# Kernel tuning notes

Hardware: AMD Instinct MI355X
Metric: run time of the kernel (lower is better)

The kernel has to match this reference:

```python
import jax, jax.numpy as jnp
import numpy as np

B, C, H, W = 4, 128, 56, 56
K = 7
K2 = K * K
RATIO = 16


def _conv1x1(x, w, b=None):
    # x: [B,C,H,W], w: [O,C]
    y = jnp.einsum('oc,bchw->bohw', w, x)
    return y if b is None else y + b[None, :, None, None]


def _dwconv(x, w, dil, pad):
    # depthwise conv, w: [C,1,k,k]
    return jax.lax.conv_general_dilated(
        x, w, window_strides=(1, 1), padding=[(pad, pad), (pad, pad)],
        rhs_dilation=(dil, dil), feature_group_count=x.shape[1],
        dimension_numbers=('NCHW', 'OIHW', 'NCHW'))


def _bn(x, s, b):
    # inference-mode BatchNorm folded to per-channel affine
    return x * s[None, :, None, None] + b[None, :, None, None]


def setup_inputs() -> dict:
    key = jax.random.key(0)
    ks = jax.random.split(key, 16)
    w = 0.05  # weight scale
    inp = {
        'x_up': jax.random.normal(ks[0], (B, C, H, W), jnp.float32),
        'x_skip': jax.random.normal(ks[1], (B, C, H, W), jnp.float32),
        'wq': jax.random.normal(ks[2], (C, C), jnp.float32) * w,
        'bq': jnp.zeros((C,), jnp.float32),
        'wk': jax.random.normal(ks[3], (C, C), jnp.float32) * w,
        'bk': jnp.zeros((C,), jnp.float32),
        'wv': jax.random.normal(ks[4], (C, C), jnp.float32) * w,
        'bv': jnp.zeros((C,), jnp.float32),
        'ww': jax.random.normal(ks[5], (K2, 49), jnp.float32) * w,
        'bw': jnp.zeros((K2,), jnp.float32),
        'lk_w': jax.random.normal(ks[6], (C, 1, K, K), jnp.float32) * 0.1,
        'lk_bn_s': jax.random.uniform(ks[7], (C,), jnp.float32, 0.5, 1.5),
        'lk_bn_b': jnp.zeros((C,), jnp.float32),
        'dw5': jax.random.normal(ks[8], (C, 1, 5, 5), jnp.float32) * 0.1,
        'bn5_s': jax.random.uniform(ks[7], (C,), jnp.float32, 0.5, 1.5),
        'bn5_b': jnp.zeros((C,), jnp.float32),
        'dw3a': jax.random.normal(ks[9], (C, 1, 3, 3), jnp.float32) * 0.1,
        'bn3a_s': jax.random.uniform(ks[9], (C,), jnp.float32, 0.5, 1.5),
        'bn3a_b': jnp.zeros((C,), jnp.float32),
        'dw3b': jax.random.normal(ks[10], (C, 1, 3, 3), jnp.float32) * 0.1,
        'bn3b_s': jax.random.uniform(ks[10], (C,), jnp.float32, 0.5, 1.5),
        'bn3b_b': jnp.zeros((C,), jnp.float32),
        'dw3c': jax.random.normal(ks[11], (C, 1, 3, 3), jnp.float32) * 0.1,
        'bn3c_s': jax.random.uniform(ks[11], (C,), jnp.float32, 0.5, 1.5),
        'bn3c_b': jnp.zeros((C,), jnp.float32),
        'lepe_bn_s': jax.random.uniform(ks[12], (C,), jnp.float32, 0.5, 1.5),
        'lepe_bn_b': jnp.zeros((C,), jnp.float32),
        'gate_w': jax.random.normal(ks[13], (C, C), jnp.float32) * w,
        'gate_bn_s': jax.random.uniform(ks[13], (C,), jnp.float32, 0.5, 1.5),
        'gate_bn_b': jnp.zeros((C,), jnp.float32),
        'fus_w': jax.random.normal(ks[14], (C, C), jnp.float32) * w,
        'fus_b': jnp.zeros((C,), jnp.float32),
        'ca_w1': jax.random.normal(ks[15], (C // RATIO, C), jnp.float32) * w,
        'ca_w2': jax.random.normal(ks[15], (C, C // RATIO), jnp.float32) * w,
        'res_scale': jnp.ones((1,), jnp.float32),
    }
    return inp


def _forward(x_up, x_skip, wq, bq, wk, bk, wv, bv, ww, bw,
             lk_w, lk_bn_s, lk_bn_b, dw5, bn5_s, bn5_b,
             dw3a, bn3a_s, bn3a_b, dw3b, bn3b_s, bn3b_b, dw3c, bn3c_s, bn3c_b,
             lepe_bn_s, lepe_bn_b, gate_w, gate_bn_s, gate_bn_b,
             fus_w, fus_b, ca_w1, ca_w2, res_scale):
    identity = x_skip

    # ---- lepe: DilatedReparamBlock (lk 7x7 dw + 4 dilated dw branches, each BN) + final BN
    out = _bn(_dwconv(x_skip, lk_w, 1, 3), lk_bn_s, lk_bn_b)
    out = out + _bn(_dwconv(x_skip, dw5, 1, 2), bn5_s, bn5_b)    # k=5, d=1
    out = out + _bn(_dwconv(x_skip, dw3a, 1, 1), bn3a_s, bn3a_b)  # k=3, d=1
    out = out + _bn(_dwconv(x_skip, dw3b, 2, 2), bn3b_s, bn3b_b)  # k=3, d=2
    out = out + _bn(_dwconv(x_skip, dw3c, 3, 3), bn3c_s, bn3c_b)  # k=3, d=3
    lepe = _bn(out, lepe_bn_s, lepe_bn_b)

    # ---- gate: 1x1 conv (no bias) -> BN -> SiLU
    gate = jax.nn.silu(_bn(_conv1x1(x_skip, gate_w), gate_bn_s, gate_bn_b))

    # ---- q / k / v
    query = _conv1x1(x_skip, wq, bq)                              # [B,C,H,W]
    # AdaptiveAvgPool2d(7): H,W divisible by 7 -> block mean
    pooled = x_up.reshape(B, C, 7, H // 7, 7, W // 7).mean(axis=(3, 5))  # [B,C,7,7]
    key_t = _conv1x1(pooled, wk, bk).reshape(B, C, 49)            # [B,C,49]
    value = _conv1x1(x_skip, wv, bv)                              # [B,C,H,W]

    # ---- attention over 49 pooled key tokens
    scale = float(C) ** -0.5
    q_r = query.reshape(B, C, H * W).transpose(0, 2, 1)           # [B,HW,C]
    attn = jax.nn.softmax(jnp.einsum('bnc,bcl->bnl', q_r, key_t) * scale, axis=-1)
    attn_r = attn.transpose(0, 2, 1).reshape(B, 49, H, W)         # [B,49,H,W]
    dyn_w = jnp.einsum('ol,blhw->bohw', ww, attn_r) + bw[None, :, None, None]  # [B,K2,H,W]

    # ---- unfold value (k=7, pad=3), torch layout: channel-major, (kh,kw) row-major
    pad = K // 2
    vp = jnp.pad(value, ((0, 0), (0, 0), (pad, pad), (pad, pad)))
    patches = jnp.stack([vp[:, :, i:i + H, j:j + W]
                         for i in range(K) for j in range(K)], axis=2)  # [B,C,K2,H,W]
    mixed = jnp.einsum('bkhw,bckhw->bchw', dyn_w, patches)

    x_fused = _conv1x1(mixed, fus_w, fus_b) + lepe

    # ---- channel attention (shared MLP on avg & max pooled)
    avg = x_fused.mean(axis=(2, 3))                               # [B,C]
    mx = x_fused.max(axis=(2, 3))                                 # [B,C]
    def ca_mlp(v):
        return jnp.einsum('cr,br->bc', ca_w2, jax.nn.relu(jnp.einsum('rc,bc->br', ca_w1, v)))
    ca = jax.nn.sigmoid(ca_mlp(avg) + ca_mlp(mx))[:, :, None, None]
    x_fused = ca * x_fused

    return gate * x_fused + identity * res_scale


def reference(x_up, x_skip, wq, bq, wk, bk, wv, bv, ww, bw,
              lk_w, lk_bn_s, lk_bn_b, dw5, bn5_s, bn5_b,
              dw3a, bn3a_s, bn3a_b, dw3b, bn3b_s, bn3b_b, dw3c, bn3c_s, bn3c_b,
              lepe_bn_s, lepe_bn_b, gate_w, gate_bn_s, gate_bn_b,
              fus_w, fus_b, ca_w1, ca_w2, res_scale):
    return _forward(x_up, x_skip, wq, bq, wk, bk, wv, bv, ww, bw,
                    lk_w, lk_bn_s, lk_bn_b, dw5, bn5_s, bn5_b,
                    dw3a, bn3a_s, bn3a_b, dw3b, bn3b_s, bn3b_b, dw3c, bn3c_s, bn3c_b,
                    lepe_bn_s, lepe_bn_b, gate_w, gate_bn_s, gate_bn_b,
                    fus_w, fus_b, ca_w1, ca_w2, res_scale)
```

## Files before the change

kernel.cpp:

```cpp
#include <hip/hip_runtime.h>

typedef unsigned int u32;

#define HW 3136
#define SCALE 0.08838834764831843f

#define OFF_W7    0
#define OFF_BIAS  6272
#define OFF_POOL  6400
#define OFF_MT    31488
#define OFF_D     56576
#define OFF_AVG   56772
#define OFF_MAXU  57284
#define OFF_CA    57796
#define OFF_WC    58308
#define OFF_BC    74692
#define OFF_FV    74820
#define OFF_GATE  1680452
#define OFF_DYN   3286084
#define OFF_XF    3900740

struct Params {
  const float *x_up, *x_skip, *wq, *bq, *wk, *bk, *wv, *bv, *ww, *bw;
  const float *lk_w, *lk_s, *lk_b, *dw5, *s5, *b5, *dw3a, *s3a, *b3a,
              *dw3b, *s3b, *b3b, *dw3c, *s3c, *b3c, *lepe_s, *lepe_b;
  const float *gate_w, *gate_s, *gate_b, *fus_w, *fus_b, *ca_w1, *ca_w2, *res;
  float* W;
  float* out;
};

__device__ __forceinline__ u32 fenc(float f){
  union{float f; u32 u;} v; v.f = f;
  return (v.u & 0x80000000u) ? ~v.u : (v.u | 0x80000000u);
}
__device__ __forceinline__ float fdec(u32 u){
  union{float f; u32 uu;} v;
  v.uu = (u & 0x80000000u) ? (u ^ 0x80000000u) : ~u;
  return v.f;
}

__global__ __launch_bounds__(256) void k_prep(Params P){
  __shared__ float pl[3136];
  __shared__ float part[208];
  float* W = P.W;
  const int tid = threadIdx.x, blk = blockIdx.x;
  if (blk < 512){
    const int b = blk >> 7, c = blk & 127;
    const float* src = P.x_up + (size_t)(b*128 + c)*HW;
    for (int idx = tid; idx < 784; idx += 256)
      *(float4*)&pl[idx*4] = *(const float4*)(src + idx*4);
    __syncthreads();
    if (tid < 196){
      const int l = tid >> 2, s = tid & 3;
      const int i = l/7, j = l%7;
      float sm = 0.f;
      #pragma unroll
      for (int r=0;r<2;++r){
        const int base = (8*i + 2*s + r)*56 + 8*j;
        #pragma unroll
        for (int e=0;e<8;++e) sm += pl[base+e];
      }
      part[tid] = sm;
    }
    __syncthreads();
    if (tid < 49){
      const float sm = part[tid*4] + part[tid*4+1] + part[tid*4+2] + part[tid*4+3];
      W[OFF_POOL + (size_t)(b*128+c)*49 + tid] = sm * (1.f/64.f);
    }
  } else if (blk < 576){
    const int o = (blk - 512)*2 + (tid >> 7), c = tid & 127;
    float a = 0.f;
    #pragma unroll 8
    for (int m=0;m<128;++m) a += P.fus_w[o*128+m] * P.wv[m*128+c];
    W[OFF_WC + o*128 + c] = a;
  } else if (blk == 576){
    for (int idx = tid; idx < 6272; idx += 256){
      const int c = idx/49, k = idx%49;
      const int dy = k/7 - 3, dx = k%7 - 3;
      float w = P.lk_s[c] * P.lk_w[c*49 + k];
      if (dy>=-2 && dy<=2 && dx>=-2 && dx<=2)
        w += P.s5[c] * P.dw5[c*25 + (dy+2)*5 + (dx+2)];
      if (dy>=-1 && dy<=1 && dx>=-1 && dx<=1)
        w += P.s3a[c] * P.dw3a[c*9 + (dy+1)*3 + (dx+1)];
      if ((dy==-2||dy==0||dy==2) && (dx==-2||dx==0||dx==2))
        w += P.s3b[c] * P.dw3b[c*9 + (dy/2+1)*3 + (dx/2+1)];
      if ((dy==-3||dy==0||dy==3) && (dx==-3||dx==0||dx==3))
        w += P.s3c[c] * P.dw3c[c*9 + (dy/3+1)*3 + (dx/3+1)];
      W[OFF_W7 + idx] = P.lepe_s[c] * w;
    }
    if (tid < 128){
      const float bs = P.lk_b[tid] + P.b5[tid] + P.b3a[tid] + P.b3b[tid] + P.b3c[tid];
      W[OFF_BIAS + tid] = P.lepe_s[tid] * bs + P.lepe_b[tid] + P.fus_b[tid];
    }
    for (int i = tid; i < 512; i += 256){
      W[OFF_AVG + i] = 0.f;
      ((u32*)W + OFF_MAXU)[i] = fenc(-1e30f);
    }
  } else {
    if (tid < 128){
      float a = 0.f;
      #pragma unroll 8
      for (int m=0;m<128;++m) a += P.fus_w[tid*128+m] * P.bv[m];
      W[OFF_BC + tid] = a;
    }
  }
}

__global__ __launch_bounds__(128) void k_key(Params P){
  __shared__ float pc[128], kc[128], red[128];
  float* W = P.W;
  const int b = blockIdx.x / 49, l = blockIdx.x % 49;
  const int t = threadIdx.x;
  pc[t] = W[OFF_POOL + (size_t)(b*128+t)*49 + l];
  __syncthreads();
  float acc = P.bk[t];
  const float4* wr = (const float4*)(P.wk + t*128);
  #pragma unroll 8
  for (int k0=0;k0<32;++k0){
    const float4 w = wr[k0];
    acc += w.x*pc[k0*4] + w.y*pc[k0*4+1] + w.z*pc[k0*4+2] + w.w*pc[k0*4+3];
  }
  kc[t] = acc;
  red[t] = P.bq[t] * acc;
  __syncthreads();
  float m = 0.f;
  #pragma unroll 8
  for (int c=0;c<128;++c) m += P.wq[c*128 + t] * kc[c];
  W[OFF_MT + (size_t)b*6272 + t*49 + l] = m * SCALE;
  if (t < 64) red[t] += red[t+64];
  __syncthreads();
  if (t < 32) red[t] += red[t+32];
  __syncthreads();
  if (t < 16) red[t] += red[t+16];
  __syncthreads();
  if (t < 8) red[t] += red[t+8];
  __syncthreads();
  if (t < 4) red[t] += red[t+4];
  __syncthreads();
  if (t == 0) W[OFF_D + b*49 + l] = (red[0]+red[1]+red[2]+red[3]) * SCALE;
}

__global__ __launch_bounds__(256) void k_gemm(Params P){
  __shared__ float xl[128][20];
  __shared__ float wl[32][133];
  float* W = P.W;
  const int tid = threadIdx.x;
  const int x = blockIdx.x, xcd = x & 7;
  const int b = xcd >> 1;
  const int p0 = ((xcd & 1) + 2*(x >> 3)) * 16;
  const int mat = blockIdx.y;
  const float* __restrict__ wsrc = mat ? P.gate_w : (W + OFF_WC);

  for (int idx = tid; idx < 512; idx += 256){
    const int c = idx >> 2, pq = idx & 3;
    *(float4*)&xl[c][pq*4] =
        *(const float4*)(P.x_skip + (size_t)(b*128+c)*HW + p0 + pq*4);
  }

  const int oq = tid >> 2, pq = tid & 3;
  const int o0 = oq*2, px = pq*4;
  float i0 = 0.f, i1 = 0.f;
  if (mat == 0){ i0 = W[OFF_BC + o0]; i1 = W[OFF_BC + o0 + 1]; }
  float a0[4], a1[4];
  #pragma unroll
  for (int j=0;j<4;++j){ a0[j]=i0; a1[j]=i1; }

  for (int g=0; g<4; ++g){
    __syncthreads();
    for (int idx = tid; idx < 1024; idx += 256){
      const int o = idx >> 3, kq = idx & 7;
      const float4 v = *(const float4*)(wsrc + (size_t)o*128 + g*32 + kq*4);
      wl[kq*4+0][o] = v.x; wl[kq*4+1][o] = v.y;
      wl[kq*4+2][o] = v.z; wl[kq*4+3][o] = v.w;
    }
    __syncthreads();
    #pragma unroll 8
    for (int k=0;k<32;++k){
      const float2 w2 = *(const float2*)&wl[k][o0];
      const float4 x4 = *(const float4*)&xl[g*32+k][px];
      const float xv[4] = {x4.x,x4.y,x4.z,x4.w};
      #pragma unroll
      for (int j=0;j<4;++j){ a0[j] += w2.x*xv[j]; a1[j] += w2.y*xv[j]; }
    }
  }
  if (mat == 0){
    float4 v0 = {a0[0],a0[1],a0[2],a0[3]};
    float4 v1 = {a1[0],a1[1],a1[2],a1[3]};
    *(float4*)(W + OFF_FV + (size_t)(b*128+o0  )*HW + p0 + px) = v0;
    *(float4*)(W + OFF_FV + (size_t)(b*128+o0+1)*HW + p0 + px) = v1;
  } else {
    const float s0 = P.gate_s[o0], s1 = P.gate_s[o0+1];
    const float c0 = P.gate_b[o0], c1 = P.gate_b[o0+1];
    #pragma unroll
    for (int j=0;j<4;++j){
      float y0 = s0*a0[j] + c0, y1 = s1*a1[j] + c1;
      a0[j] = y0 / (1.f + __expf(-y0));
      a1[j] = y1 / (1.f + __expf(-y1));
    }
    float4 v0 = {a0[0],a0[1],a0[2],a0[3]};
    float4 v1 = {a1[0],a1[1],a1[2],a1[3]};
    *(float4*)(W + OFF_GATE + (size_t)(b*128+o0  )*HW + p0 + px) = v0;
    *(float4*)(W + OFF_GATE + (size_t)(b*128+o0+1)*HW + p0 + px) = v1;
  }
}

__global__ __launch_bounds__(256) void k_attn(Params P){
  __shared__ float xl[128][16];
  __shared__ float mtl[6272];
  __shared__ float wwl[2401];
  __shared__ float attl[16][52];
  __shared__ float dvl[52];
  float* W = P.W;
  const int tid = threadIdx.x;
  const int x = blockIdx.x, xcd = x & 7;
  const int b = xcd >> 1;
  const int p0 = ((xcd & 1) + 2*(x >> 3)) * 16;

  for (int idx = tid; idx < 512; idx += 256){
    const int c = idx >> 2, pq = idx & 3;
    *(float4*)&xl[c][pq*4] =
        *(const float4*)(P.x_skip + (size_t)(b*128+c)*HW + p0 + pq*4);
  }
  for (int idx = tid; idx < 1568; idx += 256)
    *(float4*)&mtl[idx*4] = *(const float4*)(W + OFF_MT + (size_t)b*6272 + idx*4);
  for (int idx = tid; idx < 600; idx += 256)
    *(float4*)&wwl[idx*4] = *(const float4*)(P.ww + idx*4);
  if (tid == 0) wwl[2400] = P.ww[2400];
  if (tid < 49) dvl[tid] = W[OFF_D + b*49 + tid];
  __syncthreads();

  const int px = tid >> 4, sub = tid & 15;
  const int l0 = sub, l1 = sub+16, l2 = sub+32, l3 = sub+48;
  const int l3c = (l3 < 49) ? l3 : 48;
  float lv0 = dvl[l0], lv1 = dvl[l1], lv2 = dvl[l2];
  float lv3 = (l3 < 49) ? dvl[l3] : -1e30f;
  float a3 = 0.f;
  #pragma unroll 4
  for (int c=0;c<128;++c){
    const float xv = xl[c][px];
    lv0 += mtl[c*49+l0]*xv;
    lv1 += mtl[c*49+l1]*xv;
    lv2 += mtl[c*49+l2]*xv;
    a3  += mtl[c*49+l3c]*xv;
  }
  if (l3 < 49) lv3 += a3;

  float m = fmaxf(fmaxf(lv0, lv1), fmaxf(lv2, lv3));
  #pragma unroll
  for (int d=1; d<16; d<<=1) m = fmaxf(m, __shfl_xor(m, d, 64));
  const float e0 = __expf(lv0-m), e1 = __expf(lv1-m), e2 = __expf(lv2-m);
  const float e3 = (l3 < 49) ? __expf(lv3-m) : 0.f;
  float s = e0+e1+e2+e3;
  #pragma unroll
  for (int d=1; d<16; d<<=1) s += __shfl_xor(s, d, 64);
  const float inv = 1.f / s;
  attl[px][l0] = e0*inv;
  attl[px][l1] = e1*inv;
  attl[px][l2] = e2*inv;
  if (l3 < 49) attl[px][l3] = e3*inv;
  __syncthreads();

  #pragma unroll
  for (int j=0;j<4;++j){
    const int oo = sub + 16*j;
    if (oo < 49){
      float a = P.bw[oo];
      #pragma unroll 7
      for (int l=0;l<49;++l) a += wwl[oo*49+l] * attl[px][l];
      W[OFF_DYN + (size_t)(b*49+oo)*HW + p0 + px] = a;
    }
  }
}

__global__ __launch_bounds__(256) void k_mix(Params P){
  __shared__ float fvs[2][20][64];
  __shared__ float xss[2][20][64];
  __shared__ float w7s[2][49];
  float* W = P.W;
  const int tid = threadIdx.x;
  const int blk = blockIdx.x, xcd = blk & 7;
  const int b = xcd >> 1;
  const int idx2 = blk >> 3;
  const int cp = idx2 >> 1;
  const int qt = (xcd & 1) + 2*(idx2 & 1);
  const int c0 = cp*2, r0 = qt*14;

  for (int idx = tid; idx < 1280; idx += 256){
    const int a2 = idx / 320;
    const int ch = a2 & 1, arr = a2 >> 1;
    const int rem = idx % 320;
    const int rr = rem >> 4, cq = rem & 15;
    const int gr = r0 - 3 + rr, gc0 = cq*4 - 4;
    float4 v = {0.f,0.f,0.f,0.f};
    if ((unsigned)gr < 56u){
      const float* src = arr ? (P.x_skip + (size_t)(b*128 + c0 + ch)*HW + gr*56)
                             : (W + OFF_FV + (size_t)(b*128 + c0 + ch)*HW + gr*56);
      if (gc0 >= 0 && gc0 + 3 < 56){
        v = *(const float4*)(src + gc0);
      } else {
        float t[4];
        #pragma unroll
        for (int e=0;e<4;++e){
          const int gc = gc0 + e;
          t[e] = ((unsigned)gc < 56u) ? src[gc] : 0.f;
        }
        v.x=t[0]; v.y=t[1]; v.z=t[2]; v.w=t[3];
      }
    }
    if (arr) *(float4*)&xss[ch][rr][cq*4] = v;
    else     *(float4*)&fvs[ch][rr][cq*4] = v;
  }
  if (tid < 98) w7s[tid/49][tid%49] = W[OFF_W7 + (c0 + tid/49)*49 + tid%49];
  __syncthreads();

  const bool act = tid < 196;
  const int row = tid / 14, q = tid % 14;
  const int q4 = q*4;
  const int grow = r0 + row;
  float acc[2][4];
  {
    const float b0 = W[OFF_BIAS + c0], b1 = W[OFF_BIAS + c0 + 1];
    #pragma unroll
    for (int e=0;e<4;++e){ acc[0][e] = b0; acc[1][e] = b1; }
  }
  if (act){
    const float* dynb = W + OFF_DYN + (size_t)b*49*HW + grow*56 + q4;
    #pragma unroll
    for (int i=0;i<7;++i){
      float4 dr[7];
      #pragma unroll
      for (int j=0;j<7;++j)
        dr[j] = *(const float4*)(dynb + (size_t)(i*7+j)*HW);
      #pragma unroll
      for (int ch=0;ch<2;++ch){
        float fw[12], xw[12];
        {
          float4 t;
          t = *(const float4*)&fvs[ch][row+i][q4];    fw[0]=t.x;fw[1]=t.y;fw[2]=t.z;fw[3]=t.w;
          t = *(const float4*)&fvs[ch][row+i][q4+4];  fw[4]=t.x;fw[5]=t.y;fw[6]=t.z;fw[7]=t.w;
          t = *(const float4*)&fvs[ch][row+i][q4+8];  fw[8]=t.x;fw[9]=t.y;fw[10]=t.z;fw[11]=t.w;
          t = *(const float4*)&xss[ch][row+i][q4];    xw[0]=t.x;xw[1]=t.y;xw[2]=t.z;xw[3]=t.w;
          t = *(const float4*)&xss[ch][row+i][q4+4];  xw[4]=t.x;xw[5]=t.y;xw[6]=t.z;xw[7]=t.w;
          t = *(const float4*)&xss[ch][row+i][q4+8];  xw[8]=t.x;xw[9]=t.y;xw[10]=t.z;xw[11]=t.w;
        }
        #pragma unroll
        for (int j=0;j<7;++j){
          const float4 dv = dr[j];
          const float wv = w7s[ch][i*7+j];
          acc[ch][0] += dv.x*fw[j+1] + wv*xw[j+1];
          acc[ch][1] += dv.y*fw[j+2] + wv*xw[j+2];
          acc[ch][2] += dv.z*fw[j+3] + wv*xw[j+3];
          acc[ch][3] += dv.w*fw[j+4] + wv*xw[j+4];
        }
      }
    }
    #pragma unroll
    for (int ch=0;ch<2;++ch){
      float4 v = {acc[ch][0], acc[ch][1], acc[ch][2], acc[ch][3]};
      *(float4*)(W + OFF_XF + (size_t)(b*128 + c0 + ch)*HW + grow*56 + q4) = v;
    }
  }
  #pragma unroll
  for (int ch=0;ch<2;++ch){
    float s = act ? (acc[ch][0]+acc[ch][1]+acc[ch][2]+acc[ch][3]) : 0.f;
    float mm = act ? fmaxf(fmaxf(acc[ch][0],acc[ch][1]),
                           fmaxf(acc[ch][2],acc[ch][3])) : -1e30f;
    #pragma unroll
    for (int d=1; d<64; d<<=1){
      s += __shfl_xor(s, d, 64);
      mm = fmaxf(mm, __shfl_xor(mm, d, 64));
    }
    if ((tid & 63) == 0){
      atomicAdd(W + OFF_AVG + b*128 + c0 + ch, s);
      atomicMax((u32*)W + OFF_MAXU + b*128 + c0 + ch, fenc(mm));
    }
  }
}

__global__ __launch_bounds__(512) void k_ca(Params P){
  __shared__ float avl[512], mxl[512], hl[64];
  float* W = P.W;
  const int tid = threadIdx.x;
  avl[tid] = W[OFF_AVG + tid] * (1.f/3136.f);
  mxl[tid] = fdec(((u32*)W + OFF_MAXU)[tid]);
  __syncthreads();
  if (tid < 64){
    const int b = tid >> 4, which = (tid >> 3) & 1, r = tid & 7;
    const float* v = (which ? mxl : avl) + b*128;
    float a = 0.f;
    const float4* wr = (const float4*)(P.ca_w1 + r*128);
    for (int k0=0;k0<32;++k0){
      const float4 w4 = wr[k0];
      a += w4.x*v[k0*4] + w4.y*v[k0*4+1] + w4.z*v[k0*4+2] + w4.w*v[k0*4+3];
    }
    hl[tid] = fmaxf(a, 0.f);
  }
  __syncthreads();
  {
    const int b = tid >> 7, c = tid & 127;
    float a = 0.f;
    #pragma unroll
    for (int r=0;r<8;++r) a += P.ca_w2[c*8+r] * (hl[b*16+r] + hl[b*16+8+r]);
    W[OFF_CA + tid] = 1.f/(1.f + __expf(-a));
  }
}

__global__ __launch_bounds__(256) void k_final(Params P){
  float* W = P.W;
  const int tid = threadIdx.x;
  const int b = blockIdx.y;
  const int ofs = blockIdx.x*1024 + tid*4;
  const int c = ofs / 3136;
  const size_t gi = (size_t)b*401408 + ofs;
  const float ca = W[OFF_CA + b*128 + c];
  const float res = P.res[0];
  const float4 gv = *(const float4*)(W + OFF_GATE + gi);
  const float4 xv = *(const float4*)(W + OFF_XF + gi);
  const float4 sk = *(const float4*)(P.x_skip + gi);
  float4 ov;
  ov.x = gv.x*xv.x*ca + sk.x*res;
  ov.y = gv.y*xv.y*ca + sk.y*res;
  ov.z = gv.z*xv.z*ca + sk.z*res;
  ov.w = gv.w*xv.w*ca + sk.w*res;
  *(float4*)(P.out + gi) = ov;
}

extern "C" void kernel_launch(void* const* d_in, const int* in_sizes, int n_in,
                              void* d_out, int out_size, void* d_ws, size_t ws_size,
                              hipStream_t stream){
  Params P;
  const float* const* in = (const float* const*)d_in;
  P.x_up = in[0];  P.x_skip = in[1]; P.wq = in[2];  P.bq = in[3];
  P.wk = in[4];    P.bk = in[5];     P.wv = in[6];  P.bv = in[7];
  P.ww = in[8];    P.bw = in[9];
  P.lk_w = in[10]; P.lk_s = in[11];  P.lk_b = in[12];
  P.dw5 = in[13];  P.s5 = in[14];    P.b5 = in[15];
  P.dw3a = in[16]; P.s3a = in[17];   P.b3a = in[18];
  P.dw3b = in[19]; P.s3b = in[20];   P.b3b = in[21];
  P.dw3c = in[22]; P.s3c = in[23];   P.b3c = in[24];
  P.lepe_s = in[25]; P.lepe_b = in[26];
  P.gate_w = in[27]; P.gate_s = in[28]; P.gate_b = in[29];
  P.fus_w = in[30];  P.fus_b = in[31];
  P.ca_w1 = in[32];  P.ca_w2 = in[33]; P.res = in[34];
  P.W = (float*)d_ws;
  P.out = (float*)d_out;

  hipLaunchKernelGGL(k_prep,  dim3(578),   dim3(256), 0, stream, P);
  hipLaunchKernelGGL(k_key,   dim3(196),   dim3(128), 0, stream, P);
  hipLaunchKernelGGL(k_gemm,  dim3(784,2), dim3(256), 0, stream, P);
  hipLaunchKernelGGL(k_attn,  dim3(784),   dim3(256), 0, stream, P);
  hipLaunchKernelGGL(k_mix,   dim3(1024),  dim3(256), 0, stream, P);
  hipLaunchKernelGGL(k_ca,    dim3(1),     dim3(512), 0, stream, P);
  hipLaunchKernelGGL(k_final, dim3(392,4), dim3(256), 0, stream, P);
}
```

Measured before the change: 268.8 us.

## Fold Wq·Wk into one matrix and recompute gate GEMM inside final kernel

Precomputes the combined Wq^T·Wk matrix and the bias cross terms in a weight-prep kernel, so the per-position key/query stage becomes a single matvec. It also moves the gate 1x1 conv plus SiLU out of the early GEMM kernel and into the final epilogue kernel. That removes a full gate tensor write and read-back through global memory. In exchange it adds one extra launch (pooling split out of prep) and puts GEMM work into the final kernel, where its tiling may differ from the old elementwise kernel.

```diff
diff --git a/kernel.cpp b/kernel.cpp
--- a/kernel.cpp
+++ b/kernel.cpp
@@ -15,10 +15,13 @@
 #define OFF_CA    57796
 #define OFF_WC    58308
 #define OFF_BC    74692
-#define OFF_FV    74820
-#define OFF_GATE  1680452
-#define OFF_DYN   3286084
-#define OFF_XF    3900740
+#define OFF_WQKT  74820
+#define OFF_DQ    91204
+#define OFF_VB    91332
+#define OFF_S0    91460
+#define OFF_FV    91464
+#define OFF_DYN   1697096
+#define OFF_XF    2311752
 
 struct Params {
   const float *x_up, *x_skip, *wq, *bq, *wk, *bk, *wv, *bv, *ww, *bw;
@@ -39,41 +42,22 @@
   return v.f;
 }
 
-__global__ __launch_bounds__(256) void k_prep(Params P){
-  __shared__ float pl[3136];
-  __shared__ float part[208];
+__global__ __launch_bounds__(256) void k_prep_w(Params P){
   float* W = P.W;
   const int tid = threadIdx.x, blk = blockIdx.x;
-  if (blk < 512){
-    const int b = blk >> 7, c = blk & 127;
-    const float* src = P.x_up + (size_t)(b*128 + c)*HW;
-    for (int idx = tid; idx < 784; idx += 256)
-      *(float4*)&pl[idx*4] = *(const float4*)(src + idx*4);
-    __syncthreads();
-    if (tid < 196){
-      const int l = tid >> 2, s = tid & 3;
-      const int i = l/7, j = l%7;
-      float sm = 0.f;
-      #pragma unroll
-      for (int r=0;r<2;++r){
-        const int base = (8*i + 2*s + r)*56 + 8*j;
-        #pragma unroll
-        for (int e=0;e<8;++e) sm += pl[base+e];
-      }
-      part[tid] = sm;
-    }
-    __syncthreads();
-    if (tid < 49){
-      const float sm = part[tid*4] + part[tid*4+1] + part[tid*4+2] + part[tid*4+3];
-      W[OFF_POOL + (size_t)(b*128+c)*49 + tid] = sm * (1.f/64.f);
-    }
-  } else if (blk < 576){
-    const int o = (blk - 512)*2 + (tid >> 7), c = tid & 127;
+  if (blk < 64){
+    const int o = blk*2 + (tid >> 7), c = tid & 127;
     float a = 0.f;
     #pragma unroll 8
     for (int m=0;m<128;++m) a += P.fus_w[o*128+m] * P.wv[m*128+c];
     W[OFF_WC + o*128 + c] = a;
-  } else if (blk == 576){
+  } else if (blk < 128){
+    const int c = (blk-64)*2 + (tid >> 7), k = tid & 127;
+    float a = 0.f;
+    #pragma unroll 8
+    for (int o=0;o<128;++o) a += P.wq[o*128+k] * P.wk[o*128+c];
+    W[OFF_WQKT + c*128 + k] = a;
+  } else if (blk == 128){
     for (int idx = tid; idx < 6272; idx += 256){
       const int c = idx/49, k = idx%49;
       const int dy = k/7 - 3, dx = k%7 - 3;
@@ -98,35 +82,67 @@
     }
   } else {
     if (tid < 128){
-      float a = 0.f;
+      float bc = 0.f, dq = 0.f, vb = 0.f;
       #pragma unroll 8
-      for (int m=0;m<128;++m) a += P.fus_w[tid*128+m] * P.bv[m];
-      W[OFF_BC + tid] = a;
-    }
-  }
-}
-
-__global__ __launch_bounds__(128) void k_key(Params P){
-  __shared__ float pc[128], kc[128], red[128];
+      for (int m=0;m<128;++m){
+        bc += P.fus_w[tid*128+m] * P.bv[m];
+        dq += P.wq[m*128+tid] * P.bk[m];
+        vb += P.bq[m] * P.wk[m*128+tid];
+      }
+      W[OFF_BC + tid] = bc;
+      W[OFF_DQ + tid] = dq;
+      W[OFF_VB + tid] = vb;
+      if (tid == 0){
+        float s = 0.f;
+        for (int m=0;m<128;++m) s += P.bq[m]*P.bk[m];
+        W[OFF_S0] = s;
+      }
+    }
+  }
+}
+
+__global__ __launch_bounds__(256) void k_pool(Params P){
+  __shared__ float pl[3136];
+  __shared__ float part[208];
+  float* W = P.W;
+  const int tid = threadIdx.x, blk = blockIdx.x;
+  const int b = blk >> 7, c = blk & 127;
+  const float* src = P.x_up + (size_t)(b*128 + c)*HW;
+  for (int idx = tid; idx < 784; idx += 256)
+    *(float4*)&pl[idx*4] = *(const float4*)(src + idx*4);
+  __syncthreads();
+  if (tid < 196){
+    const int l = tid >> 2, s = tid & 3;
+    const int i = l/7, j = l%7;
+    float sm = 0.f;
+    #pragma unroll
+    for (int r=0;r<2;++r){
+      const int base = (8*i + 2*s + r)*56 + 8*j;
+      #pragma unroll
+      for (int e=0;e<8;++e) sm += pl[base+e];
+    }
+    part[tid] = sm;
+  }
+  __syncthreads();
+  if (tid < 49){
+    const float sm = part[tid*4] + part[tid*4+1] + part[tid*4+2] + part[tid*4+3];
+    W[OFF_POOL + (size_t)(b*128+c)*49 + tid] = sm * (1.f/64.f);
+  }
+}
+
+__global__ __launch_bounds__(128) void k_mt(Params P){
+  __shared__ float pc[128], red[128];
   float* W = P.W;
   const int b = blockIdx.x / 49, l = blockIdx.x % 49;
   const int t = threadIdx.x;
   pc[t] = W[OFF_POOL + (size_t)(b*128+t)*49 + l];
   __syncthreads();
-  float acc = P.bk[t];
-  const float4* wr = (const float4*)(P.wk + t*128);
+  float acc = W[OFF_DQ + t];
   #pragma unroll 8
-  for (int k0=0;k0<32;++k0){
-    const float4 w = wr[k0];
-    acc += w.x*pc[k0*4] + w.y*pc[k0*4+1] + w.z*pc[k0*4+2] + w.w*pc[k0*4+3];
-  }
-  kc[t] = acc;
-  red[t] = P.bq[t] * acc;
-  __syncthreads();
-  float m = 0.f;
-  #pragma unroll 8
-  for (int c=0;c<128;++c) m += P.wq[c*128 + t] * kc[c];
-  W[OFF_MT + (size_t)b*6272 + t*49 + l] = m * SCALE;
+  for (int c=0;c<128;++c) acc += W[OFF_WQKT + c*128 + t] * pc[c];
+  W[OFF_MT + (size_t)b*6272 + t*49 + l] = acc * SCALE;
+  red[t] = W[OFF_VB + t] * pc[t];
+  __syncthreads();
   if (t < 64) red[t] += red[t+64];
   __syncthreads();
   if (t < 32) red[t] += red[t+32];
@@ -137,7 +153,8 @@
   __syncthreads();
   if (t < 4) red[t] += red[t+4];
   __syncthreads();
-  if (t == 0) W[OFF_D + b*49 + l] = (red[0]+red[1]+red[2]+red[3]) * SCALE;
+  if (t == 0)
+    W[OFF_D + b*49 + l] = (red[0]+red[1]+red[2]+red[3] + W[OFF_S0]) * SCALE;
 }
 
 __global__ __launch_bounds__(256) void k_gemm(Params P){
@@ -148,8 +165,7 @@
   const int x = blockIdx.x, xcd = x & 7;
   const int b = xcd >> 1;
   const int p0 = ((xcd & 1) + 2*(x >> 3)) * 16;
-  const int mat = blockIdx.y;
-  const float* __restrict__ wsrc = mat ? P.gate_w : (W + OFF_WC);
+  const float* __restrict__ wsrc = W + OFF_WC;
 
   for (int idx = tid; idx < 512; idx += 256){
     const int c = idx >> 2, pq = idx & 3;
@@ -159,8 +175,7 @@
 
   const int oq = tid >> 2, pq = tid & 3;
   const int o0 = oq*2, px = pq*4;
-  float i0 = 0.f, i1 = 0.f;
-  if (mat == 0){ i0 = W[OFF_BC + o0]; i1 = W[OFF_BC + o0 + 1]; }
+  const float i0 = W[OFF_BC + o0], i1 = W[OFF_BC + o0 + 1];
   float a0[4], a1[4];
   #pragma unroll
   for (int j=0;j<4;++j){ a0[j]=i0; a1[j]=i1; }
@@ -183,25 +198,10 @@
       for (int j=0;j<4;++j){ a0[j] += w2.x*xv[j]; a1[j] += w2.y*xv[j]; }
     }
   }
-  if (mat == 0){
-    float4 v0 = {a0[0],a0[1],a0[2],a0[3]};
-    float4 v1 = {a1[0],a1[1],a1[2],a1[3]};
-    *(float4*)(W + OFF_FV + (size_t)(b*128+o0  )*HW + p0 + px) = v0;
-    *(float4*)(W + OFF_FV + (size_t)(b*128+o0+1)*HW + p0 + px) = v1;
-  } else {
-    const float s0 = P.gate_s[o0], s1 = P.gate_s[o0+1];
-    const float c0 = P.gate_b[o0], c1 = P.gate_b[o0+1];
-    #pragma unroll
-    for (int j=0;j<4;++j){
-      float y0 = s0*a0[j] + c0, y1 = s1*a1[j] + c1;
-      a0[j] = y0 / (1.f + __expf(-y0));
-      a1[j] = y1 / (1.f + __expf(-y1));
-    }
-    float4 v0 = {a0[0],a0[1],a0[2],a0[3]};
-    float4 v1 = {a1[0],a1[1],a1[2],a1[3]};
-    *(float4*)(W + OFF_GATE + (size_t)(b*128+o0  )*HW + p0 + px) = v0;
-    *(float4*)(W + OFF_GATE + (size_t)(b*128+o0+1)*HW + p0 + px) = v1;
-  }
+  float4 v0 = {a0[0],a0[1],a0[2],a0[3]};
+  float4 v1 = {a1[0],a1[1],a1[2],a1[3]};
+  *(float4*)(W + OFF_FV + (size_t)(b*128+o0  )*HW + p0 + px) = v0;
+  *(float4*)(W + OFF_FV + (size_t)(b*128+o0+1)*HW + p0 + px) = v1;
 }
 
 __global__ __launch_bounds__(256) void k_attn(Params P){
@@ -406,23 +406,69 @@
 }
 
 __global__ __launch_bounds__(256) void k_final(Params P){
+  __shared__ float xl[128][20];
+  __shared__ float wl[32][133];
   float* W = P.W;
   const int tid = threadIdx.x;
-  const int b = blockIdx.y;
-  const int ofs = blockIdx.x*1024 + tid*4;
-  const int c = ofs / 3136;
-  const size_t gi = (size_t)b*401408 + ofs;
-  const float ca = W[OFF_CA + b*128 + c];
+  const int x = blockIdx.x, xcd = x & 7;
+  const int b = xcd >> 1;
+  const int p0 = ((xcd & 1) + 2*(x >> 3)) * 16;
+
+  for (int idx = tid; idx < 512; idx += 256){
+    const int c = idx >> 2, pq = idx & 3;
+    *(float4*)&xl[c][pq*4] =
+        *(const float4*)(P.x_skip + (size_t)(b*128+c)*HW + p0 + pq*4);
+  }
+
+  const int oq = tid >> 2, pq = tid & 3;
+  const int o0 = oq*2, px = pq*4;
+  float a0[4] = {0.f,0.f,0.f,0.f}, a1[4] = {0.f,0.f,0.f,0.f};
+
+  for (int g=0; g<4; ++g){
+    __syncthreads();
+    for (int idx = tid; idx < 1024; idx += 256){
+      const int o = idx >> 3, kq = idx & 7;
+      const float4 v = *(const float4*)(P.gate_w + (size_t)o*128 + g*32 + kq*4);
+      wl[kq*4+0][o] = v.x; wl[kq*4+1][o] = v.y;
+      wl[kq*4+2][o] = v.z; wl[kq*4+3][o] = v.w;
+    }
+    __syncthreads();
+    #pragma unroll 8
+    for (int k=0;k<32;++k){
+      const float2 w2 = *(const float2*)&wl[k][o0];
+      const float4 x4 = *(const float4*)&xl[g*32+k][px];
+      const float xv[4] = {x4.x,x4.y,x4.z,x4.w};
+      #pragma unroll
+      for (int j=0;j<4;++j){ a0[j] += w2.x*xv[j]; a1[j] += w2.y*xv[j]; }
+    }
+  }
+  const float s0 = P.gate_s[o0], s1 = P.gate_s[o0+1];
+  const float c0 = P.gate_b[o0], c1 = P.gate_b[o0+1];
+  const float ca0 = W[OFF_CA + b*128 + o0], ca1 = W[OFF_CA + b*128 + o0 + 1];
   const float res = P.res[0];
-  const float4 gv = *(const float4*)(W + OFF_GATE + gi);
-  const float4 xv = *(const float4*)(W + OFF_XF + gi);
-  const float4 sk = *(const float4*)(P.x_skip + gi);
-  float4 ov;
-  ov.x = gv.x*xv.x*ca + sk.x*res;
-  ov.y = gv.y*xv.y*ca + sk.y*res;
-  ov.z = gv.z*xv.z*ca + sk.z*res;
-  ov.w = gv.w*xv.w*ca + sk.w*res;
-  *(float4*)(P.out + gi) = ov;
+  const float4 xf0 = *(const float4*)(W + OFF_XF + (size_t)(b*128+o0  )*HW + p0 + px);
+  const float4 xf1 = *(const float4*)(W + OFF_XF + (size_t)(b*128+o0+1)*HW + p0 + px);
+  const float4 sk0 = *(const float4*)&xl[o0][px];
+  const float4 sk1 = *(const float4*)&xl[o0+1][px];
+  float g0[4] = {a0[0],a0[1],a0[2],a0[3]};
+  float g1[4] = {a1[0],a1[1],a1[2],a1[3]};
+  #pragma unroll
+  for (int j=0;j<4;++j){
+    float y0 = s0*g0[j] + c0, y1 = s1*g1[j] + c1;
+    g0[j] = y0 / (1.f + __expf(-y0));
+    g1[j] = y1 / (1.f + __expf(-y1));
+  }
+  float4 o0v, o1v;
+  o0v.x = g0[0]*ca0*xf0.x + sk0.x*res;
+  o0v.y = g0[1]*ca0*xf0.y + sk0.y*res;
+  o0v.z = g0[2]*ca0*xf0.z + sk0.z*res;
+  o0v.w = g0[3]*ca0*xf0.w + sk0.w*res;
+  o1v.x = g1[0]*ca1*xf1.x + sk1.x*res;
+  o1v.y = g1[1]*ca1*xf1.y + sk1.y*res;
+  o1v.z = g1[2]*ca1*xf1.z + sk1.z*res;
+  o1v.w = g1[3]*ca1*xf1.w + sk1.w*res;
+  *(float4*)(P.out + (size_t)(b*128+o0  )*HW + p0 + px) = o0v;
+  *(float4*)(P.out + (size_t)(b*128+o0+1)*HW + p0 + px) = o1v;
 }
 
 extern "C" void kernel_launch(void* const* d_in, const int* in_sizes, int n_in,
@@ -445,11 +491,12 @@
   P.W = (float*)d_ws;
   P.out = (float*)d_out;
 
-  hipLaunchKernelGGL(k_prep,  dim3(578),   dim3(256), 0, stream, P);
-  hipLaunchKernelGGL(k_key,   dim3(196),   dim3(128), 0, stream, P);
-  hipLaunchKernelGGL(k_gemm,  dim3(784,2), dim3(256), 0, stream, P);
-  hipLaunchKernelGGL(k_attn,  dim3(784),   dim3(256), 0, stream, P);
-  hipLaunchKernelGGL(k_mix,   dim3(1024),  dim3(256), 0, stream, P);
-  hipLaunchKernelGGL(k_ca,    dim3(1),     dim3(512), 0, stream, P);
-  hipLaunchKernelGGL(k_final, dim3(392,4), dim3(256), 0, stream, P);
-}
+  hipLaunchKernelGGL(k_prep_w, dim3(130), dim3(256), 0, stream, P);
+  hipLaunchKernelGGL(k_pool,   dim3(512), dim3(256), 0, stream, P);
+  hipLaunchKernelGGL(k_mt,     dim3(196), dim3(128), 0, stream, P);
+  hipLaunchKernelGGL(k_gemm,   dim3(784), dim3(256), 0, stream, P);
+  hipLaunchKernelGGL(k_attn,   dim3(784), dim3(256), 0, stream, P);
+  hipLaunchKernelGGL(k_mix,    dim3(1024),dim3(256), 0, stream, P);
+  hipLaunchKernelGGL(k_ca,     dim3(1),   dim3(512), 0, stream, P);
+  hipLaunchKernelGGL(k_final,  dim3(784), dim3(256), 0, stream, P);
+}
```

Result: no change. 272.2 us (+1.3%).
